# Kernel optimization log

Measured on AMD Instinct MI355X. Metric: run time of the kernel, lower is better.

## Reference

```python
import jax, jax.numpy as jnp
from jax import lax
import numpy as np

N = 2000            # number of RPN proposals
NUM_CLASSES = 21    # Pascal-VOC classes (incl. background, as the original loops all classes)
MAX_PER_CLASS = 50
MAX_PER_IMAGE = 100
IOU_THR = 0.7
NEG = jnp.float32(-1e9)


def setup_inputs() -> dict:
    key = jax.random.key(0)
    k1, k2, k3, k4 = jax.random.split(key, 4)
    # valid [y1, x1, y2, x2] proposals inside a ~600x600 image
    yx = jax.random.uniform(k1, (N, 2), dtype=jnp.float32) * 600.0
    hw = jax.random.uniform(k2, (N, 2), dtype=jnp.float32) * 120.0 + 16.0
    rpn_proposals_bboxes = jnp.concatenate([yx, yx + hw], axis=1)
    roi_bboxes_txtytwth = jax.random.normal(k3, (N, 4), dtype=jnp.float32) * 0.1
    roi_score = jax.random.uniform(k4, (N, NUM_CLASSES), dtype=jnp.float32)
    return {
        "rpn_proposals_bboxes": rpn_proposals_bboxes,
        "roi_bboxes_txtytwth": roi_bboxes_txtytwth,
        "roi_score": roi_score,
    }


def _decode_bbox(props, deltas):
    h = props[:, 2] - props[:, 0]
    w = props[:, 3] - props[:, 1]
    cy = props[:, 0] + 0.5 * h
    cx = props[:, 1] + 0.5 * w
    dy, dx, dh, dw = deltas[:, 0], deltas[:, 1], deltas[:, 2], deltas[:, 3]
    pcy = dy * h + cy
    pcx = dx * w + cx
    ph = h * jnp.exp(dh)
    pw = w * jnp.exp(dw)
    return jnp.stack([pcy - 0.5 * ph, pcx - 0.5 * pw, pcy + 0.5 * ph, pcx + 0.5 * pw], axis=1)


def _pairwise_iou(boxes):
    # boxes: [N,4] -> iou [N,N]
    y1, x1, y2, x2 = boxes[:, 0], boxes[:, 1], boxes[:, 2], boxes[:, 3]
    area = (y2 - y1) * (x2 - x1)                      # [N]
    iy1 = jnp.maximum(y1[:, None], y1[None, :])
    ix1 = jnp.maximum(x1[:, None], x1[None, :])
    iy2 = jnp.minimum(y2[:, None], y2[None, :])
    ix2 = jnp.minimum(x2[:, None], x2[None, :])
    inter = jnp.maximum(iy2 - iy1, 0.0) * jnp.maximum(ix2 - ix1, 0.0)
    union = area[:, None] + area[None, :] - inter
    return inter / jnp.maximum(union, 1e-8)


def _nms_keep(iou_sorted):
    # iou_sorted: [N,N] IoU among boxes already sorted by descending score.
    # Greedy NMS: box i kept iff no earlier kept box overlaps it > IOU_THR.
    def body(kept, xs):
        row, i = xs                                    # row: iou of box i vs all
        suppressed = jnp.any(kept & (row > IOU_THR))
        kept = kept.at[i].set(~suppressed)
        return kept, None
    kept, _ = lax.scan(body, jnp.zeros((N,), dtype=bool), (iou_sorted, jnp.arange(N)))
    return kept


def reference(rpn_proposals_bboxes, roi_bboxes_txtytwth, roi_score):
    final_bboxes = _decode_bbox(rpn_proposals_bboxes, roi_bboxes_txtytwth)   # [N,4]
    iou = _pairwise_iou(final_bboxes)                                        # [N,N]

    # per-class descending score order
    order = jnp.argsort(-roi_score.T, axis=1)                                # [C,N]
    scores_sorted = jnp.take_along_axis(roi_score.T, order, axis=1)          # [C,N]
    # reorder IoU per class: [C,N,N]
    iou_sorted = jax.vmap(lambda o: iou[o][:, o])(order)
    kept = jax.vmap(_nms_keep)(iou_sorted)                                   # [C,N] bool
    # cap at MAX_PER_CLASS kept boxes per class (NMS max_output_size)
    rank = jnp.cumsum(kept.astype(jnp.int32), axis=1)
    valid = kept & (rank <= MAX_PER_CLASS)
    masked_scores = jnp.where(valid, scores_sorted, NEG)                     # [C,N]

    boxes_sorted = final_bboxes[order]                                       # [C,N,4]
    cls_ids = jnp.broadcast_to(jnp.arange(NUM_CLASSES, dtype=jnp.int32)[:, None], (NUM_CLASSES, N))

    # global top-k over all surviving (class, box) pairs
    flat_scores = masked_scores.reshape(-1)                                  # [C*N]
    _, idx = lax.top_k(flat_scores, MAX_PER_IMAGE)
    out_bboxes = boxes_sorted.reshape(-1, 4)[idx]                            # [K,4]
    out_cls = cls_ids.reshape(-1)[idx]                                       # [K]
    return out_bboxes, out_cls
```

## Files before the change

### kernel.cpp

```cpp
#include <hip/hip_runtime.h>

#define N 2000
#define NCLS 21
#define MAXPC 50
#define MAXPI 100
#define IOU_THR 0.7f
#define NEGV -1000000000.0f

typedef unsigned long long u64;
typedef unsigned int u32;

__device__ __forceinline__ u32 sortable(float s) {
    u32 u = __float_as_uint(s);
    return ((int)u < 0) ? ~u : (u | 0x80000000u);
}

__device__ __forceinline__ float4 decode_one(const float* __restrict__ rpn,
                                             const float* __restrict__ deltas, int i) {
    float4 p = ((const float4*)rpn)[i];
    float4 d = ((const float4*)deltas)[i];
    float h = p.z - p.x, w = p.w - p.y;
    float cy = p.x + 0.5f * h, cx = p.y + 0.5f * w;
    float pcy = d.x * h + cy;
    float pcx = d.y * w + cx;
    float ph = h * expf(d.z);
    float pw = w * expf(d.w);
    return make_float4(pcy - 0.5f * ph, pcx - 0.5f * pw, pcy + 0.5f * ph, pcx + 0.5f * pw);
}

__global__ void sort_kernel(const float* __restrict__ score, int* __restrict__ order) {
    __shared__ __align__(16) u64 skey[N];
    int c = blockIdx.x;
    for (int i = threadIdx.x; i < N; i += blockDim.x) {
        u32 u = sortable(score[i * NCLS + c]);
        skey[i] = ((u64)u << 32) | (u32)(~i);
    }
    __syncthreads();
    int i = blockIdx.y * 64 + (threadIdx.x >> 2);
    int q = threadIdx.x & 3;
    if (i < N) {
        u64 ki = skey[i];
        const ulonglong2* s2 = (const ulonglong2*)skey;
        int r = 0;
        int jj0 = q * 250;
#pragma unroll 4
        for (int jj = jj0; jj < jj0 + 250; jj++) {
            ulonglong2 v = s2[jj];
            r += (v.x > ki);
            r += (v.y > ki);
        }
        r += __shfl_xor(r, 1);
        r += __shfl_xor(r, 2);
        if (q == 0) order[c * N + r] = i;
    }
}

__global__ void nms_kernel(const float* __restrict__ rpn,
                           const float* __restrict__ deltas,
                           const int* __restrict__ order,
                           const float* __restrict__ score,
                           int* __restrict__ keep_pos,
                           int* __restrict__ keep_cnt,
                           u64* __restrict__ cand_key) {
    __shared__ float4 kbox[MAXPC];
    int c = blockIdx.x;
    int lane = threadIdx.x;
    int nk = 0;
    const int NCH = (N + 63) / 64;
    for (int chunk = 0; chunk < NCH && nk < MAXPC; chunk++) {
        __syncthreads();
        int pos = chunk * 64 + lane;
        bool valid = pos < N;
        int oi = valid ? order[c * N + pos] : 0;
        float4 b = decode_one(rpn, deltas, oi);
        float ar = (b.z - b.x) * (b.w - b.y);
        bool sup = !valid;
        for (int k = 0; k < nk; k++) {
            float4 kb = kbox[k];
            float ka = (kb.z - kb.x) * (kb.w - kb.y);
            float iy1 = fmaxf(b.x, kb.x), ix1 = fmaxf(b.y, kb.y);
            float iy2 = fminf(b.z, kb.z), ix2 = fminf(b.w, kb.w);
            float inter = fmaxf(iy2 - iy1, 0.f) * fmaxf(ix2 - ix1, 0.f);
            float iou = inter / fmaxf(ar + ka - inter, 1e-8f);
            sup = sup || (iou > IOU_THR);
        }
        u64 alive = __ballot(!sup);
        while (alive && nk < MAXPC) {
            int l = __ffsll((unsigned long long)alive) - 1;
            if (lane == l) {
                kbox[nk] = b;
                keep_pos[c * MAXPC + nk] = pos;
                u32 u = sortable(score[oi * NCLS + c]);
                cand_key[c * MAXPC + nk] = ((u64)u << 32) | (u32)(~(c * N + pos));
            }
            float bxx = __shfl(b.x, l), bxy = __shfl(b.y, l);
            float bxz = __shfl(b.z, l), bxw = __shfl(b.w, l);
            nk++;
            if (lane > l && !sup) {
                float ka = (bxz - bxx) * (bxw - bxy);
                float iy1 = fmaxf(b.x, bxx), ix1 = fmaxf(b.y, bxy);
                float iy2 = fminf(b.z, bxz), ix2 = fminf(b.w, bxw);
                float inter = fmaxf(iy2 - iy1, 0.f) * fmaxf(ix2 - ix1, 0.f);
                float iou = inter / fmaxf(ar + ka - inter, 1e-8f);
                if (iou > IOU_THR) sup = true;
            }
            u64 nb = __ballot(!sup);
            alive = (l >= 63) ? 0ull : (nb & (~0ull << (l + 1)));
        }
    }
    if (lane == 0) keep_cnt[c] = nk;
}

__global__ void topk_kernel(const float* __restrict__ rpn,
                            const float* __restrict__ deltas,
                            const int* __restrict__ order,
                            const int* __restrict__ keep_pos,
                            const int* __restrict__ keep_cnt,
                            const u64* __restrict__ cand_key,
                            float* __restrict__ out) {
    __shared__ u64 keys[NCLS][MAXPC];
    __shared__ int cnt[NCLS];
    int c = blockIdx.x;
    int lane = threadIdx.x;
    for (int t = lane; t < NCLS * MAXPC; t += 64)
        keys[t / MAXPC][t % MAXPC] = cand_key[t];
    if (lane < NCLS) cnt[lane] = keep_cnt[lane];
    __syncthreads();

    int M = 0;
#pragma unroll
    for (int cc = 0; cc < NCLS; cc++) M += cnt[cc];

    if (lane < cnt[c]) {
        u64 ki = keys[c][lane];
        int r = lane;
#pragma unroll
        for (int cc = 0; cc < NCLS; cc++) {
            if (cc == c) continue;
            int lo = 0, hi = cnt[cc];
            while (lo < hi) {
                int mid = (lo + hi) >> 1;
                if (keys[cc][mid] > ki) lo = mid + 1; else hi = mid;
            }
            r += lo;
        }
        if (r < MAXPI) {
            int flat = (int)(~(u32)ki);
            int pos = flat - c * N;
            int oi = order[c * N + pos];
            float4 b = decode_one(rpn, deltas, oi);
            out[r * 4 + 0] = b.x;
            out[r * 4 + 1] = b.y;
            out[r * 4 + 2] = b.z;
            out[r * 4 + 3] = b.w;
            out[4 * MAXPI + r] = (float)c;
        }
    }

    if (c == 0 && lane == 0 && M < MAXPI) {
        int m = M;
        int cnt0 = cnt[0];
        for (int pos = 0; pos < 150 && m < MAXPI; pos++) {
            bool valid = false;
            for (int k = 0; k < cnt0; k++)
                if (keep_pos[k] == pos) { valid = true; break; }
            if (!valid) {
                int oi = order[pos];
                float4 b = decode_one(rpn, deltas, oi);
                out[m * 4 + 0] = b.x;
                out[m * 4 + 1] = b.y;
                out[m * 4 + 2] = b.z;
                out[m * 4 + 3] = b.w;
                out[4 * MAXPI + m] = 0.0f;
                m++;
            }
        }
    }
}

extern "C" void kernel_launch(void* const* d_in, const int* in_sizes, int n_in,
                              void* d_out, int out_size, void* d_ws, size_t ws_size,
                              hipStream_t stream) {
    const float* rpn    = (const float*)d_in[0];
    const float* deltas = (const float*)d_in[1];
    const float* score  = (const float*)d_in[2];
    float* out = (float*)d_out;

    char* ws = (char*)d_ws;
    int*   order    = (int*)(ws);
    u64*   candk    = (u64*)(ws + 168000);
    int*   keep_pos = (int*)(ws + 176400);
    int*   keep_cnt = (int*)(ws + 180600);

    sort_kernel<<<dim3(NCLS, 32), 256, 0, stream>>>(score, order);
    nms_kernel<<<NCLS, 64, 0, stream>>>(rpn, deltas, order, score, keep_pos, keep_cnt, candk);
    topk_kernel<<<NCLS, 64, 0, stream>>>(rpn, deltas, order, keep_pos, keep_cnt, candk, out);
}
```

Measured before the change: 48.49 us.

## Fuse sort, NMS and top-k into one cooperative kernel with grid syncs

Merges the three kernel launches into one cooperative kernel of 672 blocks that uses grid-wide syncs between the rank-sort, per-class NMS and global top-k phases. The NMS phase also keeps kept boxes in registers distributed across lanes and reads them with shuffles instead of shared memory. The aim is to remove launch overhead and inter-kernel gaps. In exchange it pays for grid.sync barriers and leaves most blocks idle during the NMS and top-k phases, and it depends on all 672 blocks being co-resident.

```diff
diff --git a/kernel.cpp b/kernel.cpp
--- a/kernel.cpp
+++ b/kernel.cpp
@@ -1,4 +1,7 @@
 #include <hip/hip_runtime.h>
+#include <hip/hip_cooperative_groups.h>
+
+namespace cg = cooperative_groups;
 
 #define N 2000
 #define NCLS 21
@@ -6,6 +9,7 @@
 #define MAXPI 100
 #define IOU_THR 0.7f
 #define NEGV -1000000000.0f
+#define NBLK (NCLS * 32)
 
 typedef unsigned long long u64;
 typedef unsigned int u32;
@@ -28,151 +32,148 @@
     return make_float4(pcy - 0.5f * ph, pcx - 0.5f * pw, pcy + 0.5f * ph, pcx + 0.5f * pw);
 }
 
-__global__ void sort_kernel(const float* __restrict__ score, int* __restrict__ order) {
-    __shared__ __align__(16) u64 skey[N];
-    int c = blockIdx.x;
-    for (int i = threadIdx.x; i < N; i += blockDim.x) {
+__device__ __forceinline__ float iou_vs(float4 b, float ar,
+                                        float kx, float ky, float kz, float kw) {
+    float ka = (kz - kx) * (kw - ky);
+    float iy1 = fmaxf(b.x, kx), ix1 = fmaxf(b.y, ky);
+    float iy2 = fminf(b.z, kz), ix2 = fminf(b.w, kw);
+    float inter = fmaxf(iy2 - iy1, 0.f) * fmaxf(ix2 - ix1, 0.f);
+    return inter / fmaxf(ar + ka - inter, 1e-8f);
+}
+
+__global__ void __launch_bounds__(256, 4)
+fused_kernel(const float* __restrict__ rpn, const float* __restrict__ deltas,
+             const float* __restrict__ score,
+             int* __restrict__ order, int* __restrict__ keep_pos,
+             int* __restrict__ keep_cnt, u64* __restrict__ cand_key,
+             float* __restrict__ out) {
+    cg::grid_group grid = cg::this_grid();
+    __shared__ __align__(16) u64 sk[N];
+    __shared__ int scnt[NCLS];
+
+    int bx = blockIdx.x;
+    int tid = threadIdx.x;
+    int c = bx >> 5;
+    int b = bx & 31;
+
+    for (int i = tid; i < N; i += 256) {
         u32 u = sortable(score[i * NCLS + c]);
-        skey[i] = ((u64)u << 32) | (u32)(~i);
+        sk[i] = ((u64)u << 32) | (u32)(~i);
     }
     __syncthreads();
-    int i = blockIdx.y * 64 + (threadIdx.x >> 2);
-    int q = threadIdx.x & 3;
-    if (i < N) {
-        u64 ki = skey[i];
-        const ulonglong2* s2 = (const ulonglong2*)skey;
-        int r = 0;
-        int jj0 = q * 250;
+    {
+        int i = b * 64 + (tid >> 2);
+        int q = tid & 3;
+        if (i < N) {
+            u64 ki = sk[i];
+            const ulonglong2* s2 = (const ulonglong2*)sk;
+            int r = 0;
+            int jj0 = q * 250;
 #pragma unroll 4
-        for (int jj = jj0; jj < jj0 + 250; jj++) {
-            ulonglong2 v = s2[jj];
-            r += (v.x > ki);
-            r += (v.y > ki);
-        }
-        r += __shfl_xor(r, 1);
-        r += __shfl_xor(r, 2);
-        if (q == 0) order[c * N + r] = i;
-    }
-}
-
-__global__ void nms_kernel(const float* __restrict__ rpn,
-                           const float* __restrict__ deltas,
-                           const int* __restrict__ order,
-                           const float* __restrict__ score,
-                           int* __restrict__ keep_pos,
-                           int* __restrict__ keep_cnt,
-                           u64* __restrict__ cand_key) {
-    __shared__ float4 kbox[MAXPC];
-    int c = blockIdx.x;
-    int lane = threadIdx.x;
-    int nk = 0;
-    const int NCH = (N + 63) / 64;
-    for (int chunk = 0; chunk < NCH && nk < MAXPC; chunk++) {
+            for (int jj = jj0; jj < jj0 + 250; jj++) {
+                ulonglong2 v = s2[jj];
+                r += (v.x > ki);
+                r += (v.y > ki);
+            }
+            r += __shfl_xor(r, 1);
+            r += __shfl_xor(r, 2);
+            if (q == 0) order[c * N + r] = i;
+        }
+    }
+    grid.sync();
+
+    if (bx < NCLS && tid < 64) {
+        int cc = bx;
+        int lane = tid;
+        float4 kb = make_float4(0.f, 0.f, 0.f, 0.f);
+        int nk = 0;
+        const int NCH = (N + 63) / 64;
+        for (int chunk = 0; chunk < NCH && nk < MAXPC; chunk++) {
+            int pos = chunk * 64 + lane;
+            bool valid = pos < N;
+            int oi = valid ? order[cc * N + pos] : 0;
+            float4 bb = decode_one(rpn, deltas, oi);
+            float ar = (bb.z - bb.x) * (bb.w - bb.y);
+            bool sup = !valid;
+            for (int k = 0; k < nk; k++) {
+                float kx = __shfl(kb.x, k), ky = __shfl(kb.y, k);
+                float kz = __shfl(kb.z, k), kw = __shfl(kb.w, k);
+                sup = sup || (iou_vs(bb, ar, kx, ky, kz, kw) > IOU_THR);
+            }
+            u64 alive = __ballot(!sup);
+            while (alive && nk < MAXPC) {
+                int l = __ffsll((unsigned long long)alive) - 1;
+                float bxx = __shfl(bb.x, l), bxy = __shfl(bb.y, l);
+                float bxz = __shfl(bb.z, l), bxw = __shfl(bb.w, l);
+                if (lane == nk) kb = make_float4(bxx, bxy, bxz, bxw);
+                if (lane == l) {
+                    keep_pos[cc * MAXPC + nk] = pos;
+                    u32 u = sortable(score[oi * NCLS + cc]);
+                    cand_key[cc * MAXPC + nk] = ((u64)u << 32) | (u32)(~(cc * N + pos));
+                }
+                nk++;
+                if (lane > l && !sup)
+                    sup = (iou_vs(bb, ar, bxx, bxy, bxz, bxw) > IOU_THR);
+                u64 nb = __ballot(!sup);
+                alive = (l >= 63) ? 0ull : (nb & (~0ull << (l + 1)));
+            }
+        }
+        if (lane == 0) keep_cnt[cc] = nk;
+    }
+    grid.sync();
+
+    if (bx < NCLS) {
+        for (int t = tid; t < NCLS * MAXPC; t += 256)
+            sk[t] = cand_key[t];
+        if (tid < NCLS) scnt[tid] = keep_cnt[tid];
         __syncthreads();
-        int pos = chunk * 64 + lane;
-        bool valid = pos < N;
-        int oi = valid ? order[c * N + pos] : 0;
-        float4 b = decode_one(rpn, deltas, oi);
-        float ar = (b.z - b.x) * (b.w - b.y);
-        bool sup = !valid;
-        for (int k = 0; k < nk; k++) {
-            float4 kb = kbox[k];
-            float ka = (kb.z - kb.x) * (kb.w - kb.y);
-            float iy1 = fmaxf(b.x, kb.x), ix1 = fmaxf(b.y, kb.y);
-            float iy2 = fminf(b.z, kb.z), ix2 = fminf(b.w, kb.w);
-            float inter = fmaxf(iy2 - iy1, 0.f) * fmaxf(ix2 - ix1, 0.f);
-            float iou = inter / fmaxf(ar + ka - inter, 1e-8f);
-            sup = sup || (iou > IOU_THR);
-        }
-        u64 alive = __ballot(!sup);
-        while (alive && nk < MAXPC) {
-            int l = __ffsll((unsigned long long)alive) - 1;
-            if (lane == l) {
-                kbox[nk] = b;
-                keep_pos[c * MAXPC + nk] = pos;
-                u32 u = sortable(score[oi * NCLS + c]);
-                cand_key[c * MAXPC + nk] = ((u64)u << 32) | (u32)(~(c * N + pos));
-            }
-            float bxx = __shfl(b.x, l), bxy = __shfl(b.y, l);
-            float bxz = __shfl(b.z, l), bxw = __shfl(b.w, l);
-            nk++;
-            if (lane > l && !sup) {
-                float ka = (bxz - bxx) * (bxw - bxy);
-                float iy1 = fmaxf(b.x, bxx), ix1 = fmaxf(b.y, bxy);
-                float iy2 = fminf(b.z, bxz), ix2 = fminf(b.w, bxw);
-                float inter = fmaxf(iy2 - iy1, 0.f) * fmaxf(ix2 - ix1, 0.f);
-                float iou = inter / fmaxf(ar + ka - inter, 1e-8f);
-                if (iou > IOU_THR) sup = true;
-            }
-            u64 nb = __ballot(!sup);
-            alive = (l >= 63) ? 0ull : (nb & (~0ull << (l + 1)));
-        }
-    }
-    if (lane == 0) keep_cnt[c] = nk;
-}
-
-__global__ void topk_kernel(const float* __restrict__ rpn,
-                            const float* __restrict__ deltas,
-                            const int* __restrict__ order,
-                            const int* __restrict__ keep_pos,
-                            const int* __restrict__ keep_cnt,
-                            const u64* __restrict__ cand_key,
-                            float* __restrict__ out) {
-    __shared__ u64 keys[NCLS][MAXPC];
-    __shared__ int cnt[NCLS];
-    int c = blockIdx.x;
-    int lane = threadIdx.x;
-    for (int t = lane; t < NCLS * MAXPC; t += 64)
-        keys[t / MAXPC][t % MAXPC] = cand_key[t];
-    if (lane < NCLS) cnt[lane] = keep_cnt[lane];
-    __syncthreads();
-
-    int M = 0;
+        int M = 0;
 #pragma unroll
-    for (int cc = 0; cc < NCLS; cc++) M += cnt[cc];
-
-    if (lane < cnt[c]) {
-        u64 ki = keys[c][lane];
-        int r = lane;
+        for (int c2 = 0; c2 < NCLS; c2++) M += scnt[c2];
+
+        int cc = bx;
+        if (tid < scnt[cc]) {
+            u64 ki = sk[cc * MAXPC + tid];
+            int r = tid;
 #pragma unroll
-        for (int cc = 0; cc < NCLS; cc++) {
-            if (cc == c) continue;
-            int lo = 0, hi = cnt[cc];
-            while (lo < hi) {
-                int mid = (lo + hi) >> 1;
-                if (keys[cc][mid] > ki) lo = mid + 1; else hi = mid;
-            }
-            r += lo;
-        }
-        if (r < MAXPI) {
-            int flat = (int)(~(u32)ki);
-            int pos = flat - c * N;
-            int oi = order[c * N + pos];
-            float4 b = decode_one(rpn, deltas, oi);
-            out[r * 4 + 0] = b.x;
-            out[r * 4 + 1] = b.y;
-            out[r * 4 + 2] = b.z;
-            out[r * 4 + 3] = b.w;
-            out[4 * MAXPI + r] = (float)c;
-        }
-    }
-
-    if (c == 0 && lane == 0 && M < MAXPI) {
-        int m = M;
-        int cnt0 = cnt[0];
-        for (int pos = 0; pos < 150 && m < MAXPI; pos++) {
-            bool valid = false;
-            for (int k = 0; k < cnt0; k++)
-                if (keep_pos[k] == pos) { valid = true; break; }
-            if (!valid) {
-                int oi = order[pos];
-                float4 b = decode_one(rpn, deltas, oi);
-                out[m * 4 + 0] = b.x;
-                out[m * 4 + 1] = b.y;
-                out[m * 4 + 2] = b.z;
-                out[m * 4 + 3] = b.w;
-                out[4 * MAXPI + m] = 0.0f;
-                m++;
+            for (int c2 = 0; c2 < NCLS; c2++) {
+                if (c2 == cc) continue;
+                int lo = 0, hi = scnt[c2];
+                while (lo < hi) {
+                    int mid = (lo + hi) >> 1;
+                    if (sk[c2 * MAXPC + mid] > ki) lo = mid + 1; else hi = mid;
+                }
+                r += lo;
+            }
+            if (r < MAXPI) {
+                int flat = (int)(~(u32)ki);
+                int pos = flat - cc * N;
+                int oi = order[cc * N + pos];
+                float4 bb = decode_one(rpn, deltas, oi);
+                out[r * 4 + 0] = bb.x;
+                out[r * 4 + 1] = bb.y;
+                out[r * 4 + 2] = bb.z;
+                out[r * 4 + 3] = bb.w;
+                out[4 * MAXPI + r] = (float)cc;
+            }
+        }
+        if (cc == 0 && tid == 0 && M < MAXPI) {
+            int m = M;
+            int cnt0 = scnt[0];
+            for (int pos = 0; pos < 150 && m < MAXPI; pos++) {
+                bool validp = false;
+                for (int k = 0; k < cnt0; k++)
+                    if (keep_pos[k] == pos) { validp = true; break; }
+                if (!validp) {
+                    int oi = order[pos];
+                    float4 bb = decode_one(rpn, deltas, oi);
+                    out[m * 4 + 0] = bb.x;
+                    out[m * 4 + 1] = bb.y;
+                    out[m * 4 + 2] = bb.z;
+                    out[m * 4 + 3] = bb.w;
+                    out[4 * MAXPI + m] = 0.0f;
+                    m++;
+                }
             }
         }
     }
@@ -192,7 +193,8 @@
     int*   keep_pos = (int*)(ws + 176400);
     int*   keep_cnt = (int*)(ws + 180600);
 
-    sort_kernel<<<dim3(NCLS, 32), 256, 0, stream>>>(score, order);
-    nms_kernel<<<NCLS, 64, 0, stream>>>(rpn, deltas, order, score, keep_pos, keep_cnt, candk);
-    topk_kernel<<<NCLS, 64, 0, stream>>>(rpn, deltas, order, keep_pos, keep_cnt, candk, out);
-}
+    void* args[] = { (void*)&rpn, (void*)&deltas, (void*)&score, (void*)&order,
+                     (void*)&keep_pos, (void*)&keep_cnt, (void*)&candk, (void*)&out };
+    hipLaunchCooperativeKernel((const void*)fused_kernel, dim3(NBLK), dim3(256),
+                               args, 0, stream);
+}
```

After: 185.2 us. 282% more time.

## Fuse sort and NMS with histogram-based partial top-candidate selection

Applied to the files above, without the earlier changes.

Sorting and NMS are merged into one 256-thread block per class. A shared-memory histogram over the high bits of the score keys picks a bucket threshold so that only about 256 top candidates are rank-sorted instead of all 2000. If the pruned set yields fewer than 50 kept boxes, the kernel falls back to a full sort. Within each 64-box chunk, NMS now builds a pairwise suppression bitmask once and resolves keeps with ballots, replacing the per-keep shuffle-and-compare loop. This removes one kernel launch and most of the sort work, at the cost of a single large-shared-memory block per class with low parallelism.

```diff
diff --git a/kernel.cpp b/kernel.cpp
--- a/kernel.cpp
+++ b/kernel.cpp
@@ -5,7 +5,8 @@
 #define MAXPC 50
 #define MAXPI 100
 #define IOU_THR 0.7f
-#define NEGV -1000000000.0f
+#define TSEL 256
+#define NBUCK 4096
 
 typedef unsigned long long u64;
 typedef unsigned int u32;
@@ -28,87 +29,164 @@
     return make_float4(pcy - 0.5f * ph, pcx - 0.5f * pw, pcy + 0.5f * ph, pcx + 0.5f * pw);
 }
 
-__global__ void sort_kernel(const float* __restrict__ score, int* __restrict__ order) {
-    __shared__ __align__(16) u64 skey[N];
-    int c = blockIdx.x;
-    for (int i = threadIdx.x; i < N; i += blockDim.x) {
+__device__ __forceinline__ float iou_vs(float4 b, float ar,
+                                        float kx, float ky, float kz, float kw) {
+    float ka = (kz - kx) * (kw - ky);
+    float iy1 = fmaxf(b.x, kx), ix1 = fmaxf(b.y, ky);
+    float iy2 = fminf(b.z, kz), ix2 = fminf(b.w, kw);
+    float inter = fmaxf(iy2 - iy1, 0.f) * fmaxf(ix2 - ix1, 0.f);
+    return inter / fmaxf(ar + ka - inter, 1e-8f);
+}
+
+__global__ void __launch_bounds__(256, 1)
+sortnms_kernel(const float* __restrict__ rpn, const float* __restrict__ deltas,
+               const float* __restrict__ score,
+               int* __restrict__ order,
+               int* __restrict__ keep_pos,
+               int* __restrict__ keep_cnt,
+               u64* __restrict__ cand_key) {
+    __shared__ u32 key[N];
+    __shared__ u32 hist[NBUCK];
+    __shared__ __align__(16) u64 cand[N + 1];
+    __shared__ int sorder[N];
+    __shared__ int pp[2][256];
+    __shared__ float4 cbox[64];
+    __shared__ float4 kbox[MAXPC];
+    __shared__ int s_bstar, s_ctot, s_cc, s_nk;
+
+    int c = blockIdx.x, tid = threadIdx.x;
+
+    for (int t = tid; t < NBUCK; t += 256) hist[t] = 0;
+    if (tid == 0) s_cc = 0;
+    __syncthreads();
+    for (int i = tid; i < N; i += 256) {
         u32 u = sortable(score[i * NCLS + c]);
-        skey[i] = ((u64)u << 32) | (u32)(~i);
-    }
-    __syncthreads();
-    int i = blockIdx.y * 64 + (threadIdx.x >> 2);
-    int q = threadIdx.x & 3;
-    if (i < N) {
-        u64 ki = skey[i];
-        const ulonglong2* s2 = (const ulonglong2*)skey;
-        int r = 0;
-        int jj0 = q * 250;
+        key[i] = u;
+        atomicAdd(&hist[u >> 20], 1);
+    }
+    __syncthreads();
+
+    {
+        int s = 0;
+        int b0 = tid * 16;
+        for (int b = b0; b < b0 + 16; b++) s += hist[b];
+        pp[0][tid] = s;
+        __syncthreads();
+        int src = 0;
+        for (int d = 1; d < 256; d <<= 1) {
+            int v = pp[src][tid] + ((tid + d < 256) ? pp[src][tid + d] : 0);
+            pp[src ^ 1][tid] = v;
+            src ^= 1;
+            __syncthreads();
+        }
+        int suf = pp[src][tid];
+        int sufn = (tid < 255) ? pp[src][tid + 1] : 0;
+        if (suf >= TSEL && sufn < TSEL) {
+            int cum = sufn;
+            int b = tid * 16 + 15;
+            for (; b >= tid * 16; b--) {
+                cum += hist[b];
+                if (cum >= TSEL) break;
+            }
+            s_bstar = b;
+            s_ctot = cum;
+        }
+    }
+    __syncthreads();
+    int bstar = s_bstar;
+    int C = s_ctot;
+
+    for (int i = tid; i < N; i += 256) {
+        u32 u = key[i];
+        if ((int)(u >> 20) >= bstar) {
+            int s = atomicAdd(&s_cc, 1);
+            cand[s] = ((u64)u << 32) | (u32)(~i);
+        }
+    }
+    __syncthreads();
+
+    bool full = false;
+    while (true) {
+        if (full) {
+            for (int i = tid; i < N; i += 256)
+                cand[i] = ((u64)key[i] << 32) | (u32)(~i);
+            C = N;
+            __syncthreads();
+        }
+        if (tid == 0 && (C & 1)) cand[C] = 0ull;
+        __syncthreads();
+        {
+            int q = tid & 3;
+            int npair = (C + 1) >> 1;
+            int qn = (npair + 3) >> 2;
+            int lo = q * qn, hi = min(lo + qn, npair);
+            const ulonglong2* c2 = (const ulonglong2*)cand;
+            for (int e = (tid >> 2); e < C; e += 64) {
+                u64 ke = cand[e];
+                int r = 0;
+                for (int p = lo; p < hi; p++) {
+                    ulonglong2 v = c2[p];
+                    r += (v.x > ke);
+                    r += (v.y > ke);
+                }
+                r += __shfl_xor(r, 1);
+                r += __shfl_xor(r, 2);
+                if (q == 0) {
+                    int i = (int)(~(u32)ke);
+                    sorder[r] = i;
+                    order[c * N + r] = i;
+                }
+            }
+        }
+        __syncthreads();
+
+        if (tid < 64) {
+            int lane = tid;
+            int nk = 0;
+            int NCH = (C + 63) >> 6;
+            for (int chunk = 0; chunk < NCH && nk < MAXPC; chunk++) {
+                int pos = chunk * 64 + lane;
+                bool valid = pos < C;
+                int oi = sorder[valid ? pos : 0];
+                float4 bb = decode_one(rpn, deltas, oi);
+                cbox[lane] = bb;
+                float ar = (bb.z - bb.x) * (bb.w - bb.y);
+                bool sup = !valid;
+                for (int k = 0; k < nk; k++) {
+                    float4 kb = kbox[k];
+                    sup = sup || (iou_vs(bb, ar, kb.x, kb.y, kb.z, kb.w) > IOU_THR);
+                }
+                u64 supby = 0;
 #pragma unroll 4
-        for (int jj = jj0; jj < jj0 + 250; jj++) {
-            ulonglong2 v = s2[jj];
-            r += (v.x > ki);
-            r += (v.y > ki);
-        }
-        r += __shfl_xor(r, 1);
-        r += __shfl_xor(r, 2);
-        if (q == 0) order[c * N + r] = i;
-    }
-}
-
-__global__ void nms_kernel(const float* __restrict__ rpn,
-                           const float* __restrict__ deltas,
-                           const int* __restrict__ order,
-                           const float* __restrict__ score,
-                           int* __restrict__ keep_pos,
-                           int* __restrict__ keep_cnt,
-                           u64* __restrict__ cand_key) {
-    __shared__ float4 kbox[MAXPC];
-    int c = blockIdx.x;
-    int lane = threadIdx.x;
-    int nk = 0;
-    const int NCH = (N + 63) / 64;
-    for (int chunk = 0; chunk < NCH && nk < MAXPC; chunk++) {
-        __syncthreads();
-        int pos = chunk * 64 + lane;
-        bool valid = pos < N;
-        int oi = valid ? order[c * N + pos] : 0;
-        float4 b = decode_one(rpn, deltas, oi);
-        float ar = (b.z - b.x) * (b.w - b.y);
-        bool sup = !valid;
-        for (int k = 0; k < nk; k++) {
-            float4 kb = kbox[k];
-            float ka = (kb.z - kb.x) * (kb.w - kb.y);
-            float iy1 = fmaxf(b.x, kb.x), ix1 = fmaxf(b.y, kb.y);
-            float iy2 = fminf(b.z, kb.z), ix2 = fminf(b.w, kb.w);
-            float inter = fmaxf(iy2 - iy1, 0.f) * fmaxf(ix2 - ix1, 0.f);
-            float iou = inter / fmaxf(ar + ka - inter, 1e-8f);
-            sup = sup || (iou > IOU_THR);
-        }
-        u64 alive = __ballot(!sup);
-        while (alive && nk < MAXPC) {
-            int l = __ffsll((unsigned long long)alive) - 1;
-            if (lane == l) {
-                kbox[nk] = b;
-                keep_pos[c * MAXPC + nk] = pos;
-                u32 u = sortable(score[oi * NCLS + c]);
-                cand_key[c * MAXPC + nk] = ((u64)u << 32) | (u32)(~(c * N + pos));
-            }
-            float bxx = __shfl(b.x, l), bxy = __shfl(b.y, l);
-            float bxz = __shfl(b.z, l), bxw = __shfl(b.w, l);
-            nk++;
-            if (lane > l && !sup) {
-                float ka = (bxz - bxx) * (bxw - bxy);
-                float iy1 = fmaxf(b.x, bxx), ix1 = fmaxf(b.y, bxy);
-                float iy2 = fminf(b.z, bxz), ix2 = fminf(b.w, bxw);
-                float inter = fmaxf(iy2 - iy1, 0.f) * fmaxf(ix2 - ix1, 0.f);
-                float iou = inter / fmaxf(ar + ka - inter, 1e-8f);
-                if (iou > IOU_THR) sup = true;
-            }
-            u64 nb = __ballot(!sup);
-            alive = (l >= 63) ? 0ull : (nb & (~0ull << (l + 1)));
-        }
-    }
-    if (lane == 0) keep_cnt[c] = nk;
+                for (int j = 0; j < 64; j++) {
+                    float4 bj = cbox[j];
+                    supby |= (u64)(iou_vs(bb, ar, bj.x, bj.y, bj.z, bj.w) > IOU_THR) << j;
+                }
+                u64 alive = __ballot(!sup);
+                for (int l = 0; l < 64 && nk < MAXPC; l++) {
+                    u64 col = __ballot((supby >> l) & 1);
+                    if ((alive >> l) & 1) {
+                        if (lane == l) {
+                            kbox[nk] = bb;
+                            keep_pos[c * MAXPC + nk] = pos;
+                            cand_key[c * MAXPC + nk] =
+                                ((u64)key[oi] << 32) | (u32)(~(c * N + pos));
+                        }
+                        nk++;
+                        alive &= ~(col & (~0ull << (l + 1)));
+                    }
+                }
+            }
+            if (lane == 0) s_nk = nk;
+        }
+        __syncthreads();
+        if (s_nk >= MAXPC || C >= N) {
+            if (tid == 0) keep_cnt[c] = s_nk;
+            break;
+        }
+        full = true;
+        __syncthreads();
+    }
 }
 
 __global__ void topk_kernel(const float* __restrict__ rpn,
@@ -161,10 +239,10 @@
         int m = M;
         int cnt0 = cnt[0];
         for (int pos = 0; pos < 150 && m < MAXPI; pos++) {
-            bool valid = false;
+            bool validp = false;
             for (int k = 0; k < cnt0; k++)
-                if (keep_pos[k] == pos) { valid = true; break; }
-            if (!valid) {
+                if (keep_pos[k] == pos) { validp = true; break; }
+            if (!validp) {
                 int oi = order[pos];
                 float4 b = decode_one(rpn, deltas, oi);
                 out[m * 4 + 0] = b.x;
@@ -192,7 +270,8 @@
     int*   keep_pos = (int*)(ws + 176400);
     int*   keep_cnt = (int*)(ws + 180600);
 
-    sort_kernel<<<dim3(NCLS, 32), 256, 0, stream>>>(score, order);
-    nms_kernel<<<NCLS, 64, 0, stream>>>(rpn, deltas, order, score, keep_pos, keep_cnt, candk);
-    topk_kernel<<<NCLS, 64, 0, stream>>>(rpn, deltas, order, keep_pos, keep_cnt, candk, out);
-}
+    sortnms_kernel<<<NCLS, 256, 0, stream>>>(rpn, deltas, score, order,
+                                             keep_pos, keep_cnt, candk);
+    topk_kernel<<<NCLS, 64, 0, stream>>>(rpn, deltas, order,
+                                         keep_pos, keep_cnt, candk, out);
+}
```

Measured after the change: 53.43 us. 1.1x slower.
